# Kernel tuning notes

Hardware: AMD Instinct MI355X
Metric: run time of the kernel (lower is better)

## Reference

```python
import math
import jax, jax.numpy as jnp
import numpy as np

B, S, D_MODEL, H = 8, 1024, 512, 8
HEAD = D_MODEL // H
MAX_REL = 16


def rel_index(length_q, length_k):
    # clipped relative-position index matrix [Lq, Lk] in [0, 2*MAX_REL]
    rq = jnp.arange(length_q)
    rk = jnp.arange(length_k)
    dist = rk[None, :] - rq[:, None]
    return jnp.clip(dist, -MAX_REL, MAX_REL) + MAX_REL


def setup_inputs() -> dict:
    key = jax.random.key(0)
    ks = jax.random.split(key, 13)
    sc = 1.0 / math.sqrt(D_MODEL)
    inp = {
        "query": jax.random.normal(ks[0], (B, S, D_MODEL), jnp.float32),
        "key": jax.random.normal(ks[1], (B, S, D_MODEL), jnp.float32),
        "value": jax.random.normal(ks[2], (B, S, D_MODEL), jnp.float32),
        "Wq": jax.random.normal(ks[3], (D_MODEL, D_MODEL), jnp.float32) * sc,
        "bq": jnp.zeros((D_MODEL,), jnp.float32),
        "Wk": jax.random.normal(ks[4], (D_MODEL, D_MODEL), jnp.float32) * sc,
        "bk": jnp.zeros((D_MODEL,), jnp.float32),
        "Wv": jax.random.normal(ks[5], (D_MODEL, D_MODEL), jnp.float32) * sc,
        "bv": jnp.zeros((D_MODEL,), jnp.float32),
        "Wo": jax.random.normal(ks[6], (D_MODEL, D_MODEL), jnp.float32) * sc,
        "bo": jnp.zeros((D_MODEL,), jnp.float32),
        "rel_k_table": jax.random.normal(ks[7], (2 * MAX_REL + 1, HEAD), jnp.float32),
        "rel_v_table": jax.random.normal(ks[8], (2 * MAX_REL + 1, HEAD), jnp.float32),
    }
    return inp


def reference(query, key, value, Wq, bq, Wk, bk, Wv, bv, Wo, bo, rel_k_table, rel_v_table):
    b, s, d = query.shape
    # input projections (torch Linear: x @ W.T + b)
    q = query @ Wq.T + bq  # [B,S,D]
    k = key @ Wk.T + bk
    v = value @ Wv.T + bv
    # split heads: [B,H,S,HEAD]
    qh = q.reshape(b, s, H, HEAD).transpose(0, 2, 1, 3)
    kh = k.reshape(b, s, H, HEAD).transpose(0, 2, 1, 3)
    vh = v.reshape(b, s, H, HEAD).transpose(0, 2, 1, 3)
    # content-content scores
    attn1 = jnp.einsum("bhqd,bhkd->bhqk", qh, kh)
    # content-position scores via gathered relative embeddings [S,S,HEAD]
    idx = rel_index(s, s)
    rk = rel_k_table[idx]
    attn2 = jnp.einsum("bhqd,qkd->bhqk", qh, rk)
    # NOTE: original code scales by sqrt(batch_size), reproduced faithfully
    scale = math.sqrt(float(B))
    attn = jax.nn.softmax((attn1 + attn2) / scale, axis=-1)
    # values: content + relative-position value term
    w1 = jnp.einsum("bhqk,bhkd->bhqd", attn, vh)
    rv = rel_v_table[idx]
    w2 = jnp.einsum("bhqk,qkd->bhqd", attn, rv)
    x = (w1 + w2).transpose(0, 2, 1, 3).reshape(b * s, d)
    return x @ Wo.T + bo
```

## Files before the change

### kernel.cpp

```cpp
#include <hip/hip_runtime.h>

typedef unsigned short u16;
typedef float f32x4 __attribute__((ext_vector_type(4)));
typedef __bf16 bf16x8 __attribute__((ext_vector_type(8)));

#define MFMA16(a, b, c) __builtin_amdgcn_mfma_f32_16x16x32_bf16((a), (b), (c), 0, 0, 0)

#define B_ 8
#define H_ 8
#define S_ 1024

__device__ __forceinline__ u16 f2bf(float f) {
  unsigned u = __float_as_uint(f);
  return (u16)((u + 0x7fffu + ((u >> 16) & 1u)) >> 16);
}
__device__ __forceinline__ unsigned cvtpk(float a, float b) {
  unsigned r;
  asm("v_cvt_pk_bf16_f32 %0, %1, %2" : "=v"(r) : "v"(a), "v"(b));
  return r;
}
__device__ __forceinline__ void gload16(const void* g, void* l) {
  __builtin_amdgcn_global_load_lds((__attribute__((address_space(1))) const void*)g,
                                   (__attribute__((address_space(3))) void*)l, 16, 0, 0);
}

__global__ void __launch_bounds__(256) convAll(const float* __restrict__ q, const float* __restrict__ k,
                                               const float* __restrict__ v, const float* __restrict__ Wq,
                                               const float* __restrict__ Wk, const float* __restrict__ Wv,
                                               const float* __restrict__ Wo, const float* __restrict__ relk,
                                               u16* __restrict__ dq, u16* __restrict__ dk, u16* __restrict__ dv,
                                               u16* __restrict__ dWq, u16* __restrict__ dWk, u16* __restrict__ dWv,
                                               u16* __restrict__ dWo, u16* __restrict__ drelk) {
  const int bid = blockIdx.x;
  const float* s; u16* d; size_t off;
  if (bid < 12288) {
    size_t i4 = (size_t)bid * 256 + threadIdx.x;
    int tsel = (int)(i4 >> 20);
    off = (i4 & 1048575) << 2;
    s = tsel == 0 ? q : (tsel == 1 ? k : v);
    d = tsel == 0 ? dq : (tsel == 1 ? dk : dv);
  } else {
    size_t i = ((size_t)(bid - 12288) * 256 + threadIdx.x) << 2;
    if (i >= 1050688) return;
    if (i < 262144)       { s = Wq; d = dWq; off = i; }
    else if (i < 524288)  { s = Wk; d = dWk; off = i - 262144; }
    else if (i < 786432)  { s = Wv; d = dWv; off = i - 524288; }
    else if (i < 1048576) { s = Wo; d = dWo; off = i - 786432; }
    else                  { s = relk; d = drelk; off = i - 1048576; }
  }
  float4 f = *(const float4*)(s + off);
  uint2 o;
  o.x = cvtpk(f.x, f.y);
  o.y = cvtpk(f.z, f.w);
  *(uint2*)(d + off) = o;
}

__global__ void __launch_bounds__(256) qkv_gemm(const u16* __restrict__ Xq, const u16* __restrict__ Xk,
                                                const u16* __restrict__ Xv, const u16* __restrict__ Wqb,
                                                const u16* __restrict__ Wkb, const u16* __restrict__ Wvb,
                                                const float* __restrict__ bq, const float* __restrict__ bk,
                                                const float* __restrict__ bv, u16* __restrict__ Qh,
                                                u16* __restrict__ Kh, u16* __restrict__ Vt) {
  __shared__ u16 As[128 * 64];
  __shared__ u16 Bs[128 * 64];
  const int seg = blockIdx.x >> 8, bid = blockIdx.x & 255;
  const u16* A = seg == 0 ? Xq : (seg == 1 ? Xk : Xv);
  const u16* W = seg == 0 ? Wqb : (seg == 1 ? Wkb : Wvb);
  const float* bias = seg == 0 ? bq : (seg == 1 ? bk : bv);
  const int tid = threadIdx.x, lane = tid & 63, wid = tid >> 6;
  const int c = lane & 15, g = lane >> 4;
  const int bm = bid >> 2, bn = bid & 3;
  const int m0 = bm << 7, n0 = bn << 7;
  const int wrow = (wid >> 1) << 6, wcol = (wid & 1) << 6;

  const f32x4 ZF = {0.f, 0.f, 0.f, 0.f};
  f32x4 acc[4][4];
#pragma unroll
  for (int i = 0; i < 4; ++i)
#pragma unroll
    for (int j = 0; j < 4; ++j) acc[i][j] = ZF;

  for (int kt = 0; kt < 512; kt += 64) {
    __syncthreads();
#pragma unroll
    for (int i = 0; i < 4; ++i) {
      int Lb = ((wid << 2) | i) << 10;
      int L = Lb + lane * 16;
      int row = L >> 7;
      int off = (L & 127) ^ ((row & 7) << 4);
      gload16((const char*)A + ((((size_t)(m0 + row)) << 9) + kt) * 2 + off, (char*)As + Lb);
      gload16((const char*)W + ((((size_t)(n0 + row)) << 9) + kt) * 2 + off, (char*)Bs + Lb);
    }
    __syncthreads();
#pragma unroll
    for (int kk = 0; kk < 2; ++kk) {
      bf16x8 af[4], bfr[4];
#pragma unroll
      for (int rt = 0; rt < 4; ++rt) {
        int row = wrow + (rt << 4) + c;
        af[rt] = *(const bf16x8*)((const char*)As + row * 128 + (((kk << 6) | (g << 4)) ^ ((row & 7) << 4)));
      }
#pragma unroll
      for (int ct = 0; ct < 4; ++ct) {
        int row = wcol + (ct << 4) + c;
        bfr[ct] = *(const bf16x8*)((const char*)Bs + row * 128 + (((kk << 6) | (g << 4)) ^ ((row & 7) << 4)));
      }
#pragma unroll
      for (int rt = 0; rt < 4; ++rt)
#pragma unroll
        for (int ct = 0; ct < 4; ++ct) acc[rt][ct] = MFMA16(af[rt], bfr[ct], acc[rt][ct]);
    }
  }

#pragma unroll
  for (int rt = 0; rt < 4; ++rt)
#pragma unroll
    for (int ct = 0; ct < 4; ++ct) {
      int n = n0 + wcol + (ct << 4) + c;
      float bv2 = bias[n];
      if (seg == 2) {
        int b2 = m0 >> 10;
        int sbase = (m0 & 1023) + wrow + (rt << 4) + (g << 2);
        int h2 = n >> 6, d2 = n & 63;
        uint2 o;
        o.x = cvtpk(acc[rt][ct][0] + bv2, acc[rt][ct][1] + bv2);
        o.y = cvtpk(acc[rt][ct][2] + bv2, acc[rt][ct][3] + bv2);
        *(uint2*)(Vt + ((((size_t)((b2 << 3) + h2) << 6) + d2) << 10) + sbase) = o;
      } else {
        u16* out = seg == 0 ? Qh : Kh;
#pragma unroll
        for (int r = 0; r < 4; ++r) {
          int m = m0 + wrow + (rt << 4) + (g << 2) + r;
          int b = m >> 10, s = m & 1023, h = n >> 6, d = n & 63;
          out[(((((size_t)(b * H_ + h)) << 10) + s) << 6) + d] = f2bf(acc[rt][ct][r] + bv2);
        }
      }
    }
}

__global__ void __launch_bounds__(256) gemm_out(const u16* __restrict__ A, const u16* __restrict__ W,
                                                const float* __restrict__ bias, float* __restrict__ out) {
  __shared__ u16 As[128 * 64];
  __shared__ u16 Bs[128 * 64];
  const int tid = threadIdx.x, lane = tid & 63, wid = tid >> 6;
  const int c = lane & 15, g = lane >> 4;
  const int bm = blockIdx.x >> 2, bn = blockIdx.x & 3;
  const int m0 = bm << 7, n0 = bn << 7;
  const int wrow = (wid >> 1) << 6, wcol = (wid & 1) << 6;

  const f32x4 ZF = {0.f, 0.f, 0.f, 0.f};
  f32x4 acc[4][4];
#pragma unroll
  for (int i = 0; i < 4; ++i)
#pragma unroll
    for (int j = 0; j < 4; ++j) acc[i][j] = ZF;

  for (int kt = 0; kt < 512; kt += 64) {
    __syncthreads();
#pragma unroll
    for (int i = 0; i < 4; ++i) {
      int Lb = ((wid << 2) | i) << 10;
      int L = Lb + lane * 16;
      int row = L >> 7;
      int off = (L & 127) ^ ((row & 7) << 4);
      gload16((const char*)A + ((((size_t)(m0 + row)) << 9) + kt) * 2 + off, (char*)As + Lb);
      gload16((const char*)W + ((((size_t)(n0 + row)) << 9) + kt) * 2 + off, (char*)Bs + Lb);
    }
    __syncthreads();
#pragma unroll
    for (int kk = 0; kk < 2; ++kk) {
      bf16x8 af[4], bfr[4];
#pragma unroll
      for (int rt = 0; rt < 4; ++rt) {
        int row = wrow + (rt << 4) + c;
        af[rt] = *(const bf16x8*)((const char*)As + row * 128 + (((kk << 6) | (g << 4)) ^ ((row & 7) << 4)));
      }
#pragma unroll
      for (int ct = 0; ct < 4; ++ct) {
        int row = wcol + (ct << 4) + c;
        bfr[ct] = *(const bf16x8*)((const char*)Bs + row * 128 + (((kk << 6) | (g << 4)) ^ ((row & 7) << 4)));
      }
#pragma unroll
      for (int rt = 0; rt < 4; ++rt)
#pragma unroll
        for (int ct = 0; ct < 4; ++ct) acc[rt][ct] = MFMA16(af[rt], bfr[ct], acc[rt][ct]);
    }
  }

#pragma unroll
  for (int rt = 0; rt < 4; ++rt)
#pragma unroll
    for (int ct = 0; ct < 4; ++ct) {
      int n = n0 + wcol + (ct << 4) + c;
      float bv = bias[n];
#pragma unroll
      for (int r = 0; r < 4; ++r) {
        int m = m0 + wrow + (rt << 4) + (g << 2) + r;
        out[(((size_t)m) << 9) + n] = acc[rt][ct][r] + bv;
      }
    }
}

__global__ void __launch_bounds__(512) flash_kernel(const u16* __restrict__ Qh, const u16* __restrict__ Kh,
                                                    const u16* __restrict__ Vt, const u16* __restrict__ relkb,
                                                    const float* __restrict__ relv, u16* __restrict__ Xout) {
  __shared__ u16 Ks[2][64 * 64];
  __shared__ u16 Vs[2][64 * 64];
  __shared__ u16 Ps[128 * 64];
  __shared__ float qrelS[128 * 34];
  __shared__ u16 Pband[128 * 32];
  __shared__ float rv32S[64];

  const int tid = threadIdx.x, lane = tid & 63, wid = tid >> 6;
  const int c = lane & 15, g = lane >> 4;
  const int swz = ((blockIdx.x & 7) << 6) | (blockIdx.x >> 3);
  const int bh = swz >> 3, qt = swz & 7;
  const int qbase = qt << 7;
  const size_t rowbase = ((size_t)bh) << 10;
  const int qloc = (wid << 4) + c;
  const float K1 = 0.51013619f;
  const float C0 = 24.0f;

  bf16x8 qa[2];
  {
    const u16* qptr = Qh + ((rowbase + qbase + qloc) << 6);
    qa[0] = *(const bf16x8*)(qptr + (g << 3));
    qa[1] = *(const bf16x8*)(qptr + 32 + (g << 3));
  }

#define STAGE(buf, kt_) do { \
    const int k64_ = (kt_) << 6; \
    int L_ = (wid << 10) + lane * 16; \
    int row_ = L_ >> 7; \
    int off_ = (L_ & 127) ^ ((row_ & 7) << 4); \
    gload16((const char*)Kh + ((rowbase + k64_ + row_) << 7) + off_, (char*)Ks[buf] + (wid << 10)); \
    gload16((const char*)Vt + ((((size_t)bh << 6) + row_) << 11) + (k64_ << 1) + off_, (char*)Vs[buf] + (wid << 10)); \
  } while (0)

  STAGE(0, 0);

  ((uint4*)Pband)[tid] = uint4{0, 0, 0, 0};
  if (tid < 64) rv32S[tid] = relv[2048 + tid];

  {
    const f32x4 ZF = {0.f, 0.f, 0.f, 0.f};
#pragma unroll
    for (int t = 0; t < 3; ++t) {
      int rr = t * 16 + c; if (rr > 32) rr = 32;
      f32x4 qr = ZF;
#pragma unroll
      for (int kk = 0; kk < 2; ++kk) {
        bf16x8 ar = *(const bf16x8*)(relkb + (rr << 6) + (kk << 5) + (g << 3));
        qr = MFMA16(ar, qa[kk], qr);
      }
#pragma unroll
      for (int j = 0; j < 4; ++j) {
        int r = t * 16 + (g << 2) + j;
        if (r < 33) qrelS[qloc * 34 + r] = qr[j] * K1 - C0;
      }
    }
  }
  __syncthreads();

  const float bias_lo = qrelS[qloc * 34 + 0];
  const float bias_hi = qrelS[qloc * 34 + 32];

  int koff[4][2], voff[4][2], poffw[4];
#pragma unroll
  for (int t = 0; t < 4; ++t) {
#pragma unroll
    for (int kk = 0; kk < 2; ++kk)
      koff[t][kk] = ((t << 4) + c) * 128 + ((((kk << 6) | (g << 4))) ^ ((c & 7) << 4));
#pragma unroll
    for (int h2 = 0; h2 < 2; ++h2)
      voff[t][h2] = ((t << 4) + c) * 128 + ((((h2 << 6) | (g << 4))) ^ ((c & 7) << 4));
    poffw[t] = qloc * 128 + (((t << 5) | (g << 3)) ^ ((c & 7) << 4));
  }
  const int pr0 = qloc * 128 + ((g << 4) ^ ((c & 7) << 4));
  const int pr1 = pr0 ^ 64;

  const f32x4 ZF = {0.f, 0.f, 0.f, 0.f};
  f32x4 acc[4] = {ZF, ZF, ZF, ZF};
  float lsum = 0.f, lowsum = 0.f, psum = 0.f;

  for (int kt = 0; kt < 16; ++kt) {
    const int cur = kt & 1;
    if (kt < 15) STAGE(cur ^ 1, kt + 1);

    f32x4 sa[4];
#pragma unroll
    for (int t = 0; t < 4; ++t) {
      sa[t] = ZF;
#pragma unroll
      for (int kk = 0; kk < 2; ++kk) {
        bf16x8 bk = *(const bf16x8*)((const char*)Ks + (cur << 13) + koff[t][kk]);
        sa[t] = MFMA16(bk, qa[kk], sa[t]);
      }
    }

    const int D0 = (kt << 6) - qbase;
    float p[4][4];
    if (D0 >= 192) {
      float s = 0.f;
#pragma unroll
      for (int t = 0; t < 4; ++t)
#pragma unroll
        for (int j = 0; j < 4; ++j) {
          float pe = __builtin_amdgcn_exp2f(fmaf(sa[t][j], K1, bias_hi));
          p[t][j] = pe; s += pe;
        }
      lsum += s;
    } else if (D0 <= -128) {
      float s = 0.f;
#pragma unroll
      for (int t = 0; t < 4; ++t)
#pragma unroll
        for (int j = 0; j < 4; ++j) {
          float pe = __builtin_amdgcn_exp2f(fmaf(sa[t][j], K1, bias_lo));
          p[t][j] = pe; s += pe;
        }
      lsum += s; lowsum += s;
    } else {
#pragma unroll
      for (int t = 0; t < 4; ++t)
#pragma unroll
        for (int j = 0; j < 4; ++j) {
          int dlt = D0 + (t << 4) + (g << 2) + j - qloc;
          int idx = dlt < -16 ? 0 : (dlt > 16 ? 32 : dlt + 16);
          float pe = __builtin_amdgcn_exp2f(fmaf(sa[t][j], K1, qrelS[qloc * 34 + idx]));
          p[t][j] = pe;
          lsum += pe;
          if (dlt <= -16) lowsum += pe;
          else if (dlt < 16) { psum += pe; Pband[(qloc << 5) + dlt + 16] = f2bf(pe); }
        }
    }

#pragma unroll
    for (int t = 0; t < 4; ++t) {
      uint2 pk;
      pk.x = cvtpk(p[t][0], p[t][1]);
      pk.y = cvtpk(p[t][2], p[t][3]);
      *(uint2*)((char*)Ps + poffw[t]) = pk;
    }
    bf16x8 pb0 = *(const bf16x8*)((const char*)Ps + pr0);
    bf16x8 pb1 = *(const bf16x8*)((const char*)Ps + pr1);
#pragma unroll
    for (int dt = 0; dt < 4; ++dt) {
      bf16x8 av0 = *(const bf16x8*)((const char*)Vs + (cur << 13) + voff[dt][0]);
      bf16x8 av1 = *(const bf16x8*)((const char*)Vs + (cur << 13) + voff[dt][1]);
      acc[dt] = MFMA16(av0, pb0, acc[dt]);
      acc[dt] = MFMA16(av1, pb1, acc[dt]);
    }
    __syncthreads();
  }

  lsum += __shfl_xor(lsum, 16);   lsum += __shfl_xor(lsum, 32);
  lowsum += __shfl_xor(lowsum, 16); lowsum += __shfl_xor(lowsum, 32);
  psum += __shfl_xor(psum, 16);   psum += __shfl_xor(psum, 32);
  const float inv = 1.f / lsum;
  const float hsum = lsum - lowsum - psum;

  if (g == 0) Pband[qloc << 5] = f2bf(lowsum);

  u16* rvT = (u16*)qrelS;
  for (int i = tid; i < 4096; i += 512) rvT[i] = f2bf(relv[((i & 31) << 6) + (i >> 5)]);
  __syncthreads();

  bf16x8 pb2 = *(const bf16x8*)((const u16*)Pband + (qloc << 5) + (g << 3));
#pragma unroll
  for (int dt = 0; dt < 4; ++dt) {
    bf16x8 av = *(const bf16x8*)(rvT + (((dt << 4) + c) << 5) + (g << 3));
    acc[dt] = MFMA16(av, pb2, acc[dt]);
  }

  const int b = bh >> 3, h = bh & 7;
  const int q = qbase + qloc;
  u16* xb = Xout + ((((size_t)b << 10) + q) << 9) + (h << 6);
#pragma unroll
  for (int dt = 0; dt < 4; ++dt) {
    int d0 = (dt << 4) + (g << 2);
    float v0 = (acc[dt][0] + hsum * rv32S[d0 + 0]) * inv;
    float v1 = (acc[dt][1] + hsum * rv32S[d0 + 1]) * inv;
    float v2 = (acc[dt][2] + hsum * rv32S[d0 + 2]) * inv;
    float v3 = (acc[dt][3] + hsum * rv32S[d0 + 3]) * inv;
    uint2 o;
    o.x = cvtpk(v0, v1);
    o.y = cvtpk(v2, v3);
    *(uint2*)(xb + d0) = o;
  }
#undef STAGE
}

extern "C" void kernel_launch(void* const* d_in, const int* in_sizes, int n_in,
                              void* d_out, int out_size, void* d_ws, size_t ws_size,
                              hipStream_t stream) {
  (void)in_sizes; (void)n_in; (void)out_size; (void)ws_size;
  const float* query = (const float*)d_in[0];
  const float* key   = (const float*)d_in[1];
  const float* value = (const float*)d_in[2];
  const float* Wq = (const float*)d_in[3];
  const float* bq = (const float*)d_in[4];
  const float* Wk = (const float*)d_in[5];
  const float* bk = (const float*)d_in[6];
  const float* Wv = (const float*)d_in[7];
  const float* bv = (const float*)d_in[8];
  const float* Wo = (const float*)d_in[9];
  const float* bo = (const float*)d_in[10];
  const float* relk = (const float*)d_in[11];
  const float* relv = (const float*)d_in[12];

  char* ws = (char*)d_ws;
  u16*   Xq    = (u16*)(ws + 0);
  u16*   Xk    = (u16*)(ws + 8388608);
  u16*   Xv    = (u16*)(ws + 16777216);
  u16*   Wqb   = (u16*)(ws + 25165824);
  u16*   Wkb   = (u16*)(ws + 25690112);
  u16*   Wvb   = (u16*)(ws + 26214400);
  u16*   Wob   = (u16*)(ws + 26738688);
  u16*   relkb = (u16*)(ws + 27262976);
  u16*   Qh    = (u16*)(ws + 27271168);
  u16*   Kh    = (u16*)(ws + 35659776);
  u16*   Vt    = (u16*)(ws + 52436992);
  u16*   Xout  = (u16*)(ws + 70262784);

  convAll<<<13315, 256, 0, stream>>>(query, key, value, Wq, Wk, Wv, Wo, relk,
                                     Xq, Xk, Xv, Wqb, Wkb, Wvb, Wob, relkb);
  qkv_gemm<<<768, 256, 0, stream>>>(Xq, Xk, Xv, Wqb, Wkb, Wvb, bq, bk, bv, Qh, Kh, Vt);
  flash_kernel<<<512, 512, 0, stream>>>(Qh, Kh, Vt, relkb, relv, Xout);
  gemm_out<<<256, 256, 0, stream>>>(Xout, Wob, bo, (float*)d_out);
}
```

Baseline: 97.12 us.

## Switch flash kernel to 32x32 MFMA with register-resident P via permlane swap

Reworks the attention kernel so each wave handles 32 query rows using 32x32x16 bf16 MFMA instead of 16x16x32. Blocks shrink to 256 threads. The softmax probabilities are now repacked in registers with v_permlane32_swap rather than round-tripping through an LDS P buffer, which removes the LDS stores and loads for P. The trade-offs are higher register pressure, fewer waves per block, and an epilogue that writes scalar bf16 values through a shared normalization table instead of vectorized stores.

```diff
diff --git a/kernel.cpp b/kernel.cpp
--- a/kernel.cpp
+++ b/kernel.cpp
@@ -2,9 +2,11 @@
 
 typedef unsigned short u16;
 typedef float f32x4 __attribute__((ext_vector_type(4)));
+typedef float f32x16 __attribute__((ext_vector_type(16)));
 typedef __bf16 bf16x8 __attribute__((ext_vector_type(8)));
 
 #define MFMA16(a, b, c) __builtin_amdgcn_mfma_f32_16x16x32_bf16((a), (b), (c), 0, 0, 0)
+#define MFMA32(a, b, c) __builtin_amdgcn_mfma_f32_32x32x16_bf16((a), (b), (c), 0, 0, 0)
 
 #define B_ 8
 #define H_ 8
@@ -18,6 +20,9 @@
   unsigned r;
   asm("v_cvt_pk_bf16_f32 %0, %1, %2" : "=v"(r) : "v"(a), "v"(b));
   return r;
+}
+__device__ __forceinline__ void plswap(unsigned& a, unsigned& b) {
+  asm("v_permlane32_swap_b32 %0, %1" : "+v"(a), "+v"(b));
 }
 __device__ __forceinline__ void gload16(const void* g, void* l) {
   __builtin_amdgcn_global_load_lds((__attribute__((address_space(1))) const void*)g,
@@ -201,192 +206,204 @@
     }
 }
 
-__global__ void __launch_bounds__(512) flash_kernel(const u16* __restrict__ Qh, const u16* __restrict__ Kh,
+__global__ void __launch_bounds__(256) flash_kernel(const u16* __restrict__ Qh, const u16* __restrict__ Kh,
                                                     const u16* __restrict__ Vt, const u16* __restrict__ relkb,
                                                     const float* __restrict__ relv, u16* __restrict__ Xout) {
   __shared__ u16 Ks[2][64 * 64];
   __shared__ u16 Vs[2][64 * 64];
-  __shared__ u16 Ps[128 * 64];
-  __shared__ float qrelS[128 * 34];
+  __shared__ float qrelS[128 * 33];
   __shared__ u16 Pband[128 * 32];
   __shared__ float rv32S[64];
+  __shared__ float2 normS[128];
 
   const int tid = threadIdx.x, lane = tid & 63, wid = tid >> 6;
-  const int c = lane & 15, g = lane >> 4;
+  const int c32 = lane & 31, hi = lane >> 5;
   const int swz = ((blockIdx.x & 7) << 6) | (blockIdx.x >> 3);
   const int bh = swz >> 3, qt = swz & 7;
   const int qbase = qt << 7;
   const size_t rowbase = ((size_t)bh) << 10;
-  const int qloc = (wid << 4) + c;
+  const int wavebase = wid << 5;
+  const int qloc = wavebase + c32;
   const float K1 = 0.51013619f;
   const float C0 = 24.0f;
 
-  bf16x8 qa[2];
-  {
-    const u16* qptr = Qh + ((rowbase + qbase + qloc) << 6);
-    qa[0] = *(const bf16x8*)(qptr + (g << 3));
-    qa[1] = *(const bf16x8*)(qptr + 32 + (g << 3));
-  }
-
 #define STAGE(buf, kt_) do { \
     const int k64_ = (kt_) << 6; \
-    int L_ = (wid << 10) + lane * 16; \
-    int row_ = L_ >> 7; \
-    int off_ = (L_ & 127) ^ ((row_ & 7) << 4); \
-    gload16((const char*)Kh + ((rowbase + k64_ + row_) << 7) + off_, (char*)Ks[buf] + (wid << 10)); \
-    gload16((const char*)Vt + ((((size_t)bh << 6) + row_) << 11) + (k64_ << 1) + off_, (char*)Vs[buf] + (wid << 10)); \
+    _Pragma("unroll") \
+    for (int i_ = 0; i_ < 2; ++i_) { \
+      int Lb_ = ((wid << 1) | i_) << 10; \
+      int L_ = Lb_ + lane * 16; \
+      int row_ = L_ >> 7; \
+      int off_ = (L_ & 127) ^ ((row_ & 7) << 4); \
+      gload16((const char*)Kh + ((rowbase + k64_ + row_) << 7) + off_, (char*)Ks[buf] + Lb_); \
+      gload16((const char*)Vt + ((((size_t)bh << 6) + row_) << 11) + (k64_ << 1) + off_, (char*)Vs[buf] + Lb_); \
+    } \
   } while (0)
 
   STAGE(0, 0);
 
   ((uint4*)Pband)[tid] = uint4{0, 0, 0, 0};
+  ((uint4*)Pband)[tid + 256] = uint4{0, 0, 0, 0};
   if (tid < 64) rv32S[tid] = relv[2048 + tid];
 
   {
-    const f32x4 ZF = {0.f, 0.f, 0.f, 0.f};
-#pragma unroll
-    for (int t = 0; t < 3; ++t) {
-      int rr = t * 16 + c; if (rr > 32) rr = 32;
-      f32x4 qr = ZF;
-#pragma unroll
-      for (int kk = 0; kk < 2; ++kk) {
-        bf16x8 ar = *(const bf16x8*)(relkb + (rr << 6) + (kk << 5) + (g << 3));
-        qr = MFMA16(ar, qa[kk], qr);
-      }
-#pragma unroll
-      for (int j = 0; j < 4; ++j) {
-        int r = t * 16 + (g << 2) + j;
-        if (r < 33) qrelS[qloc * 34 + r] = qr[j] * K1 - C0;
-      }
-    }
-  }
+    const int c = lane & 15, g = lane >> 4;
+    const f32x4 ZF4 = {0.f, 0.f, 0.f, 0.f};
+#pragma unroll
+    for (int hf = 0; hf < 2; ++hf) {
+      const int q16 = wavebase + (hf << 4) + c;
+      const u16* qp = Qh + ((rowbase + qbase + q16) << 6);
+      bf16x8 qa0 = *(const bf16x8*)(qp + (g << 3));
+      bf16x8 qa1 = *(const bf16x8*)(qp + 32 + (g << 3));
+#pragma unroll
+      for (int t = 0; t < 3; ++t) {
+        int rr = t * 16 + c; if (rr > 32) rr = 32;
+        f32x4 qr = ZF4;
+        qr = MFMA16(*(const bf16x8*)(relkb + (rr << 6) + (g << 3)), qa0, qr);
+        qr = MFMA16(*(const bf16x8*)(relkb + (rr << 6) + 32 + (g << 3)), qa1, qr);
+#pragma unroll
+        for (int j = 0; j < 4; ++j) {
+          int r = t * 16 + (g << 2) + j;
+          if (r < 33) qrelS[q16 * 33 + r] = qr[j] * K1 - C0;
+        }
+      }
+    }
+  }
+
+  bf16x8 qb[4];
+  {
+    const u16* qp = Qh + ((rowbase + qbase + qloc) << 6);
+#pragma unroll
+    for (int ks = 0; ks < 4; ++ks) qb[ks] = *(const bf16x8*)(qp + (ks << 4) + (hi << 3));
+  }
+
   __syncthreads();
 
-  const float bias_lo = qrelS[qloc * 34 + 0];
-  const float bias_hi = qrelS[qloc * 34 + 32];
-
-  int koff[4][2], voff[4][2], poffw[4];
-#pragma unroll
-  for (int t = 0; t < 4; ++t) {
-#pragma unroll
-    for (int kk = 0; kk < 2; ++kk)
-      koff[t][kk] = ((t << 4) + c) * 128 + ((((kk << 6) | (g << 4))) ^ ((c & 7) << 4));
-#pragma unroll
-    for (int h2 = 0; h2 < 2; ++h2)
-      voff[t][h2] = ((t << 4) + c) * 128 + ((((h2 << 6) | (g << 4))) ^ ((c & 7) << 4));
-    poffw[t] = qloc * 128 + (((t << 5) | (g << 3)) ^ ((c & 7) << 4));
-  }
-  const int pr0 = qloc * 128 + ((g << 4) ^ ((c & 7) << 4));
-  const int pr1 = pr0 ^ 64;
-
-  const f32x4 ZF = {0.f, 0.f, 0.f, 0.f};
-  f32x4 acc[4] = {ZF, ZF, ZF, ZF};
+  const float bias_lo = qrelS[qloc * 33 + 0];
+  const float bias_hi = qrelS[qloc * 33 + 32];
+
+  int off2[2][4];
+#pragma unroll
+  for (int mt = 0; mt < 2; ++mt) {
+    int row = (mt << 5) + c32;
+#pragma unroll
+    for (int ks = 0; ks < 4; ++ks)
+      off2[mt][ks] = row * 128 + ((((ks << 5) | (hi << 4))) ^ ((row & 7) << 4));
+  }
+
+  const f32x16 Z16 = {0.f,0.f,0.f,0.f,0.f,0.f,0.f,0.f,0.f,0.f,0.f,0.f,0.f,0.f,0.f,0.f};
+  f32x16 acc0 = Z16, acc1 = Z16;
   float lsum = 0.f, lowsum = 0.f, psum = 0.f;
 
   for (int kt = 0; kt < 16; ++kt) {
     const int cur = kt & 1;
     if (kt < 15) STAGE(cur ^ 1, kt + 1);
 
-    f32x4 sa[4];
-#pragma unroll
-    for (int t = 0; t < 4; ++t) {
-      sa[t] = ZF;
-#pragma unroll
-      for (int kk = 0; kk < 2; ++kk) {
-        bf16x8 bk = *(const bf16x8*)((const char*)Ks + (cur << 13) + koff[t][kk]);
-        sa[t] = MFMA16(bk, qa[kk], sa[t]);
-      }
+    f32x16 sA = Z16, sB = Z16;
+#pragma unroll
+    for (int ks = 0; ks < 4; ++ks) {
+      bf16x8 ka0 = *(const bf16x8*)((const char*)Ks + (cur << 13) + off2[0][ks]);
+      bf16x8 ka1 = *(const bf16x8*)((const char*)Ks + (cur << 13) + off2[1][ks]);
+      sA = MFMA32(ka0, qb[ks], sA);
+      sB = MFMA32(ka1, qb[ks], sB);
     }
 
     const int D0 = (kt << 6) - qbase;
-    float p[4][4];
     if (D0 >= 192) {
-      float s = 0.f;
-#pragma unroll
-      for (int t = 0; t < 4; ++t)
-#pragma unroll
-        for (int j = 0; j < 4; ++j) {
-          float pe = __builtin_amdgcn_exp2f(fmaf(sa[t][j], K1, bias_hi));
-          p[t][j] = pe; s += pe;
-        }
-      lsum += s;
+      float t0 = 0.f;
+#pragma unroll
+      for (int r = 0; r < 16; ++r) {
+        float pe = __builtin_amdgcn_exp2f(fmaf(sA[r], K1, bias_hi)); sA[r] = pe; t0 += pe;
+        float pf = __builtin_amdgcn_exp2f(fmaf(sB[r], K1, bias_hi)); sB[r] = pf; t0 += pf;
+      }
+      lsum += t0;
     } else if (D0 <= -128) {
-      float s = 0.f;
-#pragma unroll
-      for (int t = 0; t < 4; ++t)
-#pragma unroll
-        for (int j = 0; j < 4; ++j) {
-          float pe = __builtin_amdgcn_exp2f(fmaf(sa[t][j], K1, bias_lo));
-          p[t][j] = pe; s += pe;
-        }
-      lsum += s; lowsum += s;
+      float t0 = 0.f;
+#pragma unroll
+      for (int r = 0; r < 16; ++r) {
+        float pe = __builtin_amdgcn_exp2f(fmaf(sA[r], K1, bias_lo)); sA[r] = pe; t0 += pe;
+        float pf = __builtin_amdgcn_exp2f(fmaf(sB[r], K1, bias_lo)); sB[r] = pf; t0 += pf;
+      }
+      lsum += t0; lowsum += t0;
     } else {
-#pragma unroll
-      for (int t = 0; t < 4; ++t)
-#pragma unroll
-        for (int j = 0; j < 4; ++j) {
-          int dlt = D0 + (t << 4) + (g << 2) + j - qloc;
+      const int base = D0 - qloc + (hi << 2);
+#pragma unroll
+      for (int mt = 0; mt < 2; ++mt) {
+        f32x16& s = mt ? sB : sA;
+#pragma unroll
+        for (int r = 0; r < 16; ++r) {
+          int dlt = base + (mt << 5) + (r & 3) + ((r >> 2) << 3);
           int idx = dlt < -16 ? 0 : (dlt > 16 ? 32 : dlt + 16);
-          float pe = __builtin_amdgcn_exp2f(fmaf(sa[t][j], K1, qrelS[qloc * 34 + idx]));
-          p[t][j] = pe;
+          float pe = __builtin_amdgcn_exp2f(fmaf(s[r], K1, qrelS[qloc * 33 + idx]));
+          s[r] = pe;
           lsum += pe;
           if (dlt <= -16) lowsum += pe;
           else if (dlt < 16) { psum += pe; Pband[(qloc << 5) + dlt + 16] = f2bf(pe); }
         }
-    }
-
-#pragma unroll
-    for (int t = 0; t < 4; ++t) {
-      uint2 pk;
-      pk.x = cvtpk(p[t][0], p[t][1]);
-      pk.y = cvtpk(p[t][2], p[t][3]);
-      *(uint2*)((char*)Ps + poffw[t]) = pk;
-    }
-    bf16x8 pb0 = *(const bf16x8*)((const char*)Ps + pr0);
-    bf16x8 pb1 = *(const bf16x8*)((const char*)Ps + pr1);
-#pragma unroll
-    for (int dt = 0; dt < 4; ++dt) {
-      bf16x8 av0 = *(const bf16x8*)((const char*)Vs + (cur << 13) + voff[dt][0]);
-      bf16x8 av1 = *(const bf16x8*)((const char*)Vs + (cur << 13) + voff[dt][1]);
-      acc[dt] = MFMA16(av0, pb0, acc[dt]);
-      acc[dt] = MFMA16(av1, pb1, acc[dt]);
+      }
+    }
+
+    unsigned uA[8], uB[8];
+#pragma unroll
+    for (int j = 0; j < 8; ++j) {
+      uA[j] = cvtpk(sA[2 * j], sA[2 * j + 1]);
+      uB[j] = cvtpk(sB[2 * j], sB[2 * j + 1]);
+    }
+    bf16x8 pa[4];
+#pragma unroll
+    for (int ks = 0; ks < 4; ++ks) {
+      int jb = (ks & 1) << 2;
+      unsigned w0, w1, w2, w3;
+      if (ks < 2) { w0 = uA[jb]; w2 = uA[jb + 2]; w1 = uA[jb + 1]; w3 = uA[jb + 3]; }
+      else        { w0 = uB[jb]; w2 = uB[jb + 2]; w1 = uB[jb + 1]; w3 = uB[jb + 3]; }
+      plswap(w0, w2);
+      plswap(w1, w3);
+      uint4 t4{w0, w1, w2, w3};
+      pa[ks] = __builtin_bit_cast(bf16x8, t4);
+    }
+
+#pragma unroll
+    for (int ks = 0; ks < 4; ++ks) {
+      bf16x8 vb0 = *(const bf16x8*)((const char*)Vs + (cur << 13) + off2[0][ks]);
+      bf16x8 vb1 = *(const bf16x8*)((const char*)Vs + (cur << 13) + off2[1][ks]);
+      acc0 = MFMA32(pa[ks], vb0, acc0);
+      acc1 = MFMA32(pa[ks], vb1, acc1);
     }
     __syncthreads();
   }
 
-  lsum += __shfl_xor(lsum, 16);   lsum += __shfl_xor(lsum, 32);
-  lowsum += __shfl_xor(lowsum, 16); lowsum += __shfl_xor(lowsum, 32);
-  psum += __shfl_xor(psum, 16);   psum += __shfl_xor(psum, 32);
+  lsum += __shfl_xor(lsum, 32);
+  lowsum += __shfl_xor(lowsum, 32);
+  psum += __shfl_xor(psum, 32);
   const float inv = 1.f / lsum;
   const float hsum = lsum - lowsum - psum;
-
-  if (g == 0) Pband[qloc << 5] = f2bf(lowsum);
-
+  if (lane < 32) {
+    Pband[qloc << 5] = f2bf(lowsum);
+    normS[qloc] = float2{inv, hsum};
+  }
+  __syncthreads();
   u16* rvT = (u16*)qrelS;
-  for (int i = tid; i < 4096; i += 512) rvT[i] = f2bf(relv[((i & 31) << 6) + (i >> 5)]);
+  for (int i = tid; i < 2048; i += 256) rvT[i] = f2bf(relv[((i & 31) << 6) + (i >> 5)]);
   __syncthreads();
 
-  bf16x8 pb2 = *(const bf16x8*)((const u16*)Pband + (qloc << 5) + (g << 3));
-#pragma unroll
-  for (int dt = 0; dt < 4; ++dt) {
-    bf16x8 av = *(const bf16x8*)(rvT + (((dt << 4) + c) << 5) + (g << 3));
-    acc[dt] = MFMA16(av, pb2, acc[dt]);
+#pragma unroll
+  for (int ks2 = 0; ks2 < 2; ++ks2) {
+    bf16x8 pf = *(const bf16x8*)(Pband + (qloc << 5) + (ks2 << 4) + (hi << 3));
+    bf16x8 rv0 = *(const bf16x8*)(rvT + (c32 << 5) + (ks2 << 4) + (hi << 3));
+    bf16x8 rv1 = *(const bf16x8*)(rvT + ((32 + c32) << 5) + (ks2 << 4) + (hi << 3));
+    acc0 = MFMA32(pf, rv0, acc0);
+    acc1 = MFMA32(pf, rv1, acc1);
   }
 
   const int b = bh >> 3, h = bh & 7;
-  const int q = qbase + qloc;
-  u16* xb = Xout + ((((size_t)b << 10) + q) << 9) + (h << 6);
-#pragma unroll
-  for (int dt = 0; dt < 4; ++dt) {
-    int d0 = (dt << 4) + (g << 2);
-    float v0 = (acc[dt][0] + hsum * rv32S[d0 + 0]) * inv;
-    float v1 = (acc[dt][1] + hsum * rv32S[d0 + 1]) * inv;
-    float v2 = (acc[dt][2] + hsum * rv32S[d0 + 2]) * inv;
-    float v3 = (acc[dt][3] + hsum * rv32S[d0 + 3]) * inv;
-    uint2 o;
-    o.x = cvtpk(v0, v1);
-    o.y = cvtpk(v2, v3);
-    *(uint2*)(xb + d0) = o;
+  const float rvA = rv32S[c32], rvB = rv32S[32 + c32];
+#pragma unroll
+  for (int r = 0; r < 16; ++r) {
+    int qw = wavebase + (r & 3) + ((r >> 2) << 3) + (hi << 2);
+    float2 nh = normS[qw];
+    size_t orow = ((((size_t)b << 10) + (qbase + qw)) << 9) + (h << 6);
+    Xout[orow + c32]      = f2bf((acc0[r] + nh.y * rvA) * nh.x);
+    Xout[orow + 32 + c32] = f2bf((acc1[r] + nh.y * rvB) * nh.x);
   }
 #undef STAGE
 }
@@ -426,6 +443,6 @@
   convAll<<<13315, 256, 0, stream>>>(query, key, value, Wq, Wk, Wv, Wo, relk,
                                      Xq, Xk, Xv, Wqb, Wkb, Wvb, Wob, relkb);
   qkv_gemm<<<768, 256, 0, stream>>>(Xq, Xk, Xv, Wqb, Wkb, Wvb, bq, bk, bv, Qh, Kh, Vt);
-  flash_kernel<<<512, 512, 0, stream>>>(Qh, Kh, Vt, relkb, relv, Xout);
+  flash_kernel<<<512, 256, 0, stream>>>(Qh, Kh, Vt, relkb, relv, Xout);
   gemm_out<<<256, 256, 0, stream>>>(Xout, Wob, bo, (float*)d_out);
 }
```

Result: slower. 102.7 us (+5.7%).
